# Kernel optimization log

Hardware: AMD Instinct MI355X
Metric: run time of the kernel (lower is better)

The kernel has to match this reference:

```python
import jax, jax.numpy as jnp
from jax import lax
import numpy as np

VOCAB, IN_DIM, MEM_DIM, SEQ = 100000, 256, 512, 2048
PAD = 0


def setup_inputs() -> dict:
    key = jax.random.key(0)
    k = jax.random.split(key, 7)
    emb = jax.random.normal(k[0], (VOCAB, IN_DIM), dtype=jnp.float32)
    emb = emb.at[PAD].set(0.0)  # padding_idx row is zero
    s_ih = 1.0 / np.sqrt(IN_DIM)
    s_hh = 1.0 / np.sqrt(MEM_DIM)
    return {
        "linputs": jax.random.randint(k[1], (SEQ,), 0, VOCAB, dtype=jnp.int64),
        "rinputs": jax.random.randint(k[2], (SEQ,), 0, VOCAB, dtype=jnp.int64),
        "emb": emb,
        "W_ih": jax.random.normal(k[3], (4 * MEM_DIM, IN_DIM), dtype=jnp.float32) * s_ih,
        "W_hh": jax.random.normal(k[4], (4 * MEM_DIM, MEM_DIM), dtype=jnp.float32) * s_hh,
        "b_ih": jax.random.normal(k[5], (4 * MEM_DIM,), dtype=jnp.float32) * s_hh,
        "b_hh": jax.random.normal(k[6], (4 * MEM_DIM,), dtype=jnp.float32) * s_hh,
    }


def _lstm_last_h(x_seq, W_ih, W_hh, b):
    # x_seq: [S, in_dim]. Returns h_T [mem_dim]. PyTorch gate order: i, f, g, o.
    H = W_hh.shape[1]
    # precompute input projections for all timesteps (one big GEMM)
    xp = x_seq @ W_ih.T + b  # [S, 4H]
    def step(carry, xg):
        h, c = carry
        gates = xg + h @ W_hh.T  # [4H]
        i = jax.nn.sigmoid(gates[:H])
        f = jax.nn.sigmoid(gates[H:2 * H])
        g = jnp.tanh(gates[2 * H:3 * H])
        o = jax.nn.sigmoid(gates[3 * H:])
        c = f * c + i * g
        h = o * jnp.tanh(c)
        return (h, c), None
    init = (jnp.zeros((H,), x_seq.dtype), jnp.zeros((H,), x_seq.dtype))
    (h, _), _ = lax.scan(step, init, xp)
    return h


def reference(linputs, rinputs, emb, W_ih, W_hh, b_ih, b_hh):
    b = b_ih + b_hh
    lx = emb[linputs]  # [S, in_dim]
    rx = emb[rinputs]
    lh = _lstm_last_h(lx, W_ih, W_hh, b)
    rh = _lstm_last_h(rx, W_ih, W_hh, b)
    return jnp.exp(-jnp.sum(jnp.abs(lh - rh)))
```

## Files before the change

kernel.cpp:

```cpp
#include <hip/hip_runtime.h>
#include <hip/hip_bf16.h>

#define SEQL  2048
#define IND   256
#define MEMD  512
#define G4    2048
#define NWG   16
#define VOCABN 100000

typedef __attribute__((ext_vector_type(4))) unsigned uintx4;

__device__ __forceinline__ unsigned short f2bf(float f) {
  unsigned u = __float_as_uint(f);
  u += 0x7fffu + ((u >> 16) & 1u);
  return (unsigned short)(u >> 16);
}
__device__ __forceinline__ float bf2f(unsigned b) {
  return __uint_as_float(b << 16);
}

template <int CTRL>
__device__ __forceinline__ float dpp_fold_add(float v) {
  int x = __builtin_amdgcn_update_dpp(0, __float_as_int(v), CTRL, 0xf, 0xf, true);
  return v + __int_as_float(x);
}

__global__ void init_k(unsigned* __restrict__ hbuf) {
  int i = blockIdx.x * blockDim.x + threadIdx.x;
  if (i < 2 * 2 * MEMD) hbuf[i] = 0u;
}

__global__ __launch_bounds__(256) void xp_gemm(
    const int* __restrict__ lin, const int* __restrict__ rin,
    const float* __restrict__ emb, const float* __restrict__ W_ih,
    const float* __restrict__ b_ih, const float* __restrict__ b_hh,
    unsigned short* __restrict__ xp) {
  __shared__ float As[64][68];
  __shared__ float Bs[64][68];
  const int s = blockIdx.z;
  const int* ids = (s == 0) ? lin : rin;
  const int t0 = blockIdx.x * 64;
  const int n0 = blockIdx.y * 64;
  const int tid = threadIdx.x;
  const int tx = tid & 15, ty = tid >> 4;

  float acc[4][4];
#pragma unroll
  for (int i = 0; i < 4; ++i)
#pragma unroll
    for (int j = 0; j < 4; ++j) acc[i][j] = 0.f;

  for (int kc = 0; kc < IND; kc += 64) {
#pragma unroll
    for (int j = 0; j < 4; ++j) {
      int fi  = tid + 256 * j;
      int row = fi >> 4;
      int c4  = fi & 15;
      int id  = ids[t0 + row];
      id = max(0, min(id, VOCABN - 1));
      const float4 va = *(const float4*)(emb + (size_t)id * IND + kc + c4 * 4);
      As[c4 * 4 + 0][row] = va.x; As[c4 * 4 + 1][row] = va.y;
      As[c4 * 4 + 2][row] = va.z; As[c4 * 4 + 3][row] = va.w;
      const float4 vb = *(const float4*)(W_ih + (size_t)(n0 + row) * IND + kc + c4 * 4);
      Bs[c4 * 4 + 0][row] = vb.x; Bs[c4 * 4 + 1][row] = vb.y;
      Bs[c4 * 4 + 2][row] = vb.z; Bs[c4 * 4 + 3][row] = vb.w;
    }
    __syncthreads();
#pragma unroll 8
    for (int k = 0; k < 64; ++k) {
      const float4 a = *(const float4*)&As[k][tx * 4];
      const float4 b = *(const float4*)&Bs[k][ty * 4];
      acc[0][0] = fmaf(a.x, b.x, acc[0][0]); acc[0][1] = fmaf(a.x, b.y, acc[0][1]);
      acc[0][2] = fmaf(a.x, b.z, acc[0][2]); acc[0][3] = fmaf(a.x, b.w, acc[0][3]);
      acc[1][0] = fmaf(a.y, b.x, acc[1][0]); acc[1][1] = fmaf(a.y, b.y, acc[1][1]);
      acc[1][2] = fmaf(a.y, b.z, acc[1][2]); acc[1][3] = fmaf(a.y, b.w, acc[1][3]);
      acc[2][0] = fmaf(a.z, b.x, acc[2][0]); acc[2][1] = fmaf(a.z, b.y, acc[2][1]);
      acc[2][2] = fmaf(a.z, b.z, acc[2][2]); acc[2][3] = fmaf(a.z, b.w, acc[2][3]);
      acc[3][0] = fmaf(a.w, b.x, acc[3][0]); acc[3][1] = fmaf(a.w, b.y, acc[3][1]);
      acc[3][2] = fmaf(a.w, b.z, acc[3][2]); acc[3][3] = fmaf(a.w, b.w, acc[3][3]);
    }
    __syncthreads();
  }
#pragma unroll
  for (int ri = 0; ri < 4; ++ri) {
#pragma unroll
    for (int bj = 0; bj < 4; ++bj) {
      int t = t0 + tx * 4 + ri;
      int n = n0 + ty * 4 + bj;
      float v = acc[ri][bj] + b_ih[n] + b_hh[n];
      int w = (n & 511) >> 5;
      int gate = n >> 9;
      int hd = n & 31;
      int pos = w * 128 + hd * 4 + gate;
      xp[((size_t)s * SEQL + t) * G4 + pos] = f2bf(v);
    }
  }
}

__global__ __launch_bounds__(512) void lstm_rec(
    const float* __restrict__ W_hh,
    const unsigned short* __restrict__ xp,
    unsigned* __restrict__ hbuf) {
  __shared__ float hlds[16 * 36];
  const int blk = blockIdx.x;
  const int s = blk & 1;
  const int w = blk >> 1;
  const int tid = threadIdx.x;
  const int lane = tid & 63;
  const int wv = tid >> 6;
  const int cg = tid & 15;
  const int rg = tid >> 4;

  float wreg[4][32];
#pragma unroll
  for (int g = 0; g < 4; ++g) {
    const float* src = W_hh + ((size_t)g * MEMD + w * 32 + rg) * MEMD + cg * 32;
#pragma unroll
    for (int q = 0; q < 8; ++q) {
      const float4 v = *(const float4*)(src + q * 4);
      wreg[g][q * 4 + 0] = v.x; wreg[g][q * 4 + 1] = v.y;
      wreg[g][q * 4 + 2] = v.z; wreg[g][q * 4 + 3] = v.w;
    }
  }

  unsigned* hbase = hbuf + s * (2 * MEMD);
  const unsigned short* xq0 = xp + (size_t)s * SEQL * G4 + w * 128 + rg * 4;
  float cst = 0.f;

  ushort4 xg_cur = *(const ushort4*)xq0;

  for (int t = 0; t < SEQL; ++t) {
    ushort4 xg_next;
    {
      int tn = (t + 1 < SEQL) ? t + 1 : t;
      xg_next = *(const ushort4*)(xq0 + (size_t)tn * G4);
    }

    if (wv == 0) {
      const unsigned* hr = hbase + (t & 1) * MEMD;
      unsigned v[8];
      const unsigned want = (unsigned)t;
      int guard = 0;
      for (;;) {
#pragma unroll
        for (int j = 0; j < 8; ++j)
          v[j] = __hip_atomic_load(hr + lane + 64 * j, __ATOMIC_RELAXED,
                                   __HIP_MEMORY_SCOPE_AGENT);
        bool good = true;
#pragma unroll
        for (int j = 0; j < 8; ++j) good &= ((v[j] >> 16) == want);
        if (__all(good)) break;
        if (++guard > (1 << 20)) break;
      }
#pragma unroll
      for (int j = 0; j < 8; ++j) {
        int wj = lane + 64 * j;
        hlds[(wj >> 5) * 36 + (wj & 31)] = bf2f(v[j] & 0xffffu);
      }
    }
    __syncthreads();

    float hreg[32];
#pragma unroll
    for (int q = 0; q < 8; ++q) {
      const float4 hv = *(const float4*)&hlds[cg * 36 + q * 4];
      hreg[q * 4 + 0] = hv.x; hreg[q * 4 + 1] = hv.y;
      hreg[q * 4 + 2] = hv.z; hreg[q * 4 + 3] = hv.w;
    }
    float part[4] = {0.f, 0.f, 0.f, 0.f};
#pragma unroll
    for (int kk = 0; kk < 32; ++kk) {
#pragma unroll
      for (int g = 0; g < 4; ++g)
        part[g] = fmaf(wreg[g][kk], hreg[kk], part[g]);
    }
#pragma unroll
    for (int g = 0; g < 4; ++g) {
      part[g] = dpp_fold_add<0xB1>(part[g]);
      part[g] = dpp_fold_add<0x4E>(part[g]);
      part[g] = dpp_fold_add<0x141>(part[g]);
      part[g] = dpp_fold_add<0x140>(part[g]);
    }

    float gi = part[0] + bf2f(xg_cur.x);
    float gf = part[1] + bf2f(xg_cur.y);
    float gg = part[2] + bf2f(xg_cur.z);
    float go = part[3] + bf2f(xg_cur.w);
    float i_ = 1.f / (1.f + __expf(-gi));
    float f_ = 1.f / (1.f + __expf(-gf));
    float ggc = fminf(fmaxf(gg, -15.f), 15.f);
    float e2 = __expf(-2.f * ggc);
    float g_ = (1.f - e2) / (1.f + e2);
    float o_ = 1.f / (1.f + __expf(-go));
    cst = f_ * cst + i_ * g_;
    float cc = fminf(fmaxf(cst, -15.f), 15.f);
    float e2c = __expf(-2.f * cc);
    float th = (1.f - e2c) / (1.f + e2c);
    float h_ = o_ * th;

    unsigned pw = (((unsigned)(t + 1)) << 16) | (unsigned)f2bf(h_);
    unsigned q1 = __shfl(pw, 16, 64);
    unsigned q2 = __shfl(pw, 32, 64);
    unsigned q3 = __shfl(pw, 48, 64);
    if (lane == 0) {
      uintx4 val;
      val.x = pw; val.y = q1; val.z = q2; val.w = q3;
      unsigned long long addr =
          (unsigned long long)(hbase + ((t + 1) & 1) * MEMD + w * 32 + wv * 4);
      asm volatile("global_store_dwordx4 %0, %1, off sc0 sc1"
                   :: "v"(addr), "v"(val) : "memory");
    }
    xg_cur = xg_next;
  }
}

__global__ __launch_bounds__(512) void finish_k(const unsigned* __restrict__ hbuf,
                                                float* __restrict__ out) {
  const int tid = threadIdx.x;
  float l = bf2f(hbuf[tid] & 0xffffu);
  float r = bf2f(hbuf[2 * MEMD + tid] & 0xffffu);
  float d = fabsf(l - r);
#pragma unroll
  for (int m = 32; m >= 1; m >>= 1) d += __shfl_xor(d, m, 64);
  __shared__ float wsum[8];
  if ((tid & 63) == 0) wsum[tid >> 6] = d;
  __syncthreads();
  if (tid == 0) {
    float sum = 0.f;
#pragma unroll
    for (int i = 0; i < 8; ++i) sum += wsum[i];
    out[0] = expf(-sum);
  }
}

extern "C" void kernel_launch(void* const* d_in, const int* in_sizes, int n_in,
                              void* d_out, int out_size, void* d_ws, size_t ws_size,
                              hipStream_t stream) {
  const int*   lin  = (const int*)d_in[0];
  const int*   rin  = (const int*)d_in[1];
  const float* emb  = (const float*)d_in[2];
  const float* W_ih = (const float*)d_in[3];
  const float* W_hh = (const float*)d_in[4];
  const float* b_ih = (const float*)d_in[5];
  const float* b_hh = (const float*)d_in[6];
  float* out = (float*)d_out;

  unsigned char* ws = (unsigned char*)d_ws;
  unsigned short* xp = (unsigned short*)ws;
  unsigned* hbuf = (unsigned*)(ws + (size_t)2 * SEQL * G4 * sizeof(unsigned short));

  hipLaunchKernelGGL(init_k, dim3(2), dim3(1024), 0, stream, hbuf);
  hipLaunchKernelGGL(xp_gemm, dim3(SEQL / 64, G4 / 64, 2), dim3(256), 0, stream,
                     lin, rin, emb, W_ih, b_ih, b_hh, xp);
  hipLaunchKernelGGL(lstm_rec, dim3(2 * NWG), dim3(512), 0, stream, W_hh, xp, hbuf);
  hipLaunchKernelGGL(finish_k, dim3(1), dim3(512), 0, stream, hbuf, out);
}
```

Baseline: 3.786 ms.

## Switch recurrent state and weights to fp16 with packed fdot2 matvec

Stores the input projections and the exchanged hidden state as fp16 instead of bf16, and packs the W_hh register slice into half2 pairs so the recurrent matvec uses v_dot2 (fdot2) with fp32 accumulation. The hidden-state poll now uses two dwordx4 loads per lane instead of eight scalar atomics. The LDS staging buffer holds packed half pairs, and launch bounds request two blocks per SM. The intent is fewer instructions and fewer registers on the serial per-step critical path, at the cost of fp16 range and precision for the weights and gate inputs.

```diff
diff --git a/kernel.cpp b/kernel.cpp
--- a/kernel.cpp
+++ b/kernel.cpp
@@ -9,14 +9,14 @@
 #define VOCABN 100000
 
 typedef __attribute__((ext_vector_type(4))) unsigned uintx4;
-
-__device__ __forceinline__ unsigned short f2bf(float f) {
-  unsigned u = __float_as_uint(f);
-  u += 0x7fffu + ((u >> 16) & 1u);
-  return (unsigned short)(u >> 16);
-}
-__device__ __forceinline__ float bf2f(unsigned b) {
-  return __uint_as_float(b << 16);
+typedef __attribute__((ext_vector_type(2))) _Float16 half2v;
+
+__device__ __forceinline__ unsigned short f2h_bits(float f) {
+  _Float16 h = (_Float16)f;
+  return __builtin_bit_cast(unsigned short, h);
+}
+__device__ __forceinline__ float h2f(unsigned bits) {
+  return (float)__builtin_bit_cast(_Float16, (unsigned short)(bits & 0xffffu));
 }
 
 template <int CTRL>
@@ -92,16 +92,16 @@
       int gate = n >> 9;
       int hd = n & 31;
       int pos = w * 128 + hd * 4 + gate;
-      xp[((size_t)s * SEQL + t) * G4 + pos] = f2bf(v);
-    }
-  }
-}
-
-__global__ __launch_bounds__(512) void lstm_rec(
+      xp[((size_t)s * SEQL + t) * G4 + pos] = f2h_bits(v);
+    }
+  }
+}
+
+__global__ __launch_bounds__(512, 2) void lstm_rec(
     const float* __restrict__ W_hh,
     const unsigned short* __restrict__ xp,
     unsigned* __restrict__ hbuf) {
-  __shared__ float hlds[16 * 36];
+  __shared__ unsigned hlds[16 * 20];
   const int blk = blockIdx.x;
   const int s = blk & 1;
   const int w = blk >> 1;
@@ -111,15 +111,17 @@
   const int cg = tid & 15;
   const int rg = tid >> 4;
 
-  float wreg[4][32];
+  half2v wreg[4][16];
 #pragma unroll
   for (int g = 0; g < 4; ++g) {
     const float* src = W_hh + ((size_t)g * MEMD + w * 32 + rg) * MEMD + cg * 32;
 #pragma unroll
     for (int q = 0; q < 8; ++q) {
       const float4 v = *(const float4*)(src + q * 4);
-      wreg[g][q * 4 + 0] = v.x; wreg[g][q * 4 + 1] = v.y;
-      wreg[g][q * 4 + 2] = v.z; wreg[g][q * 4 + 3] = v.w;
+      half2v p0; p0.x = (_Float16)v.x; p0.y = (_Float16)v.y;
+      half2v p1; p1.x = (_Float16)v.z; p1.y = (_Float16)v.w;
+      wreg[g][q * 2 + 0] = p0;
+      wreg[g][q * 2 + 1] = p1;
     }
   }
 
@@ -137,42 +139,54 @@
     }
 
     if (wv == 0) {
-      const unsigned* hr = hbase + (t & 1) * MEMD;
-      unsigned v[8];
+      const unsigned* hr = hbase + (t & 1) * MEMD + 8 * lane;
+      unsigned long long a0 = (unsigned long long)hr;
+      unsigned long long a1 = (unsigned long long)(hr + 4);
+      uintx4 va, vb;
       const unsigned want = (unsigned)t;
       int guard = 0;
       for (;;) {
-#pragma unroll
-        for (int j = 0; j < 8; ++j)
-          v[j] = __hip_atomic_load(hr + lane + 64 * j, __ATOMIC_RELAXED,
-                                   __HIP_MEMORY_SCOPE_AGENT);
-        bool good = true;
-#pragma unroll
-        for (int j = 0; j < 8; ++j) good &= ((v[j] >> 16) == want);
+        asm volatile(
+            "global_load_dwordx4 %0, %2, off sc0 sc1\n\t"
+            "global_load_dwordx4 %1, %3, off sc0 sc1\n\t"
+            "s_waitcnt vmcnt(0)"
+            : "=&v"(va), "=&v"(vb)
+            : "v"(a0), "v"(a1)
+            : "memory");
+        bool good = (va.x >> 16) == want && (va.y >> 16) == want &&
+                    (va.z >> 16) == want && (va.w >> 16) == want &&
+                    (vb.x >> 16) == want && (vb.y >> 16) == want &&
+                    (vb.z >> 16) == want && (vb.w >> 16) == want;
         if (__all(good)) break;
-        if (++guard > (1 << 20)) break;
+        if (++guard > (1 << 16)) break;
       }
-#pragma unroll
-      for (int j = 0; j < 8; ++j) {
-        int wj = lane + 64 * j;
-        hlds[(wj >> 5) * 36 + (wj & 31)] = bf2f(v[j] & 0xffffu);
+      uintx4 pk;
+      pk.x = (va.x & 0xffffu) | (va.y << 16);
+      pk.y = (va.z & 0xffffu) | (va.w << 16);
+      pk.z = (vb.x & 0xffffu) | (vb.y << 16);
+      pk.w = (vb.z & 0xffffu) | (vb.w << 16);
+      *(uintx4*)&hlds[(lane >> 2) * 20 + (lane & 3) * 4] = pk;
+    }
+    __syncthreads();
+
+    half2v hp[16];
+    {
+      const uintx4* hq = (const uintx4*)&hlds[cg * 20];
+#pragma unroll
+      for (int q = 0; q < 4; ++q) {
+        uintx4 u = hq[q];
+        hp[q * 4 + 0] = __builtin_bit_cast(half2v, u.x);
+        hp[q * 4 + 1] = __builtin_bit_cast(half2v, u.y);
+        hp[q * 4 + 2] = __builtin_bit_cast(half2v, u.z);
+        hp[q * 4 + 3] = __builtin_bit_cast(half2v, u.w);
       }
     }
-    __syncthreads();
-
-    float hreg[32];
-#pragma unroll
-    for (int q = 0; q < 8; ++q) {
-      const float4 hv = *(const float4*)&hlds[cg * 36 + q * 4];
-      hreg[q * 4 + 0] = hv.x; hreg[q * 4 + 1] = hv.y;
-      hreg[q * 4 + 2] = hv.z; hreg[q * 4 + 3] = hv.w;
-    }
     float part[4] = {0.f, 0.f, 0.f, 0.f};
 #pragma unroll
-    for (int kk = 0; kk < 32; ++kk) {
+    for (int p = 0; p < 16; ++p) {
 #pragma unroll
       for (int g = 0; g < 4; ++g)
-        part[g] = fmaf(wreg[g][kk], hreg[kk], part[g]);
+        part[g] = __builtin_amdgcn_fdot2(wreg[g][p], hp[p], part[g], false);
     }
 #pragma unroll
     for (int g = 0; g < 4; ++g) {
@@ -182,10 +196,10 @@
       part[g] = dpp_fold_add<0x140>(part[g]);
     }
 
-    float gi = part[0] + bf2f(xg_cur.x);
-    float gf = part[1] + bf2f(xg_cur.y);
-    float gg = part[2] + bf2f(xg_cur.z);
-    float go = part[3] + bf2f(xg_cur.w);
+    float gi = part[0] + h2f(xg_cur.x);
+    float gf = part[1] + h2f(xg_cur.y);
+    float gg = part[2] + h2f(xg_cur.z);
+    float go = part[3] + h2f(xg_cur.w);
     float i_ = 1.f / (1.f + __expf(-gi));
     float f_ = 1.f / (1.f + __expf(-gf));
     float ggc = fminf(fmaxf(gg, -15.f), 15.f);
@@ -198,7 +212,7 @@
     float th = (1.f - e2c) / (1.f + e2c);
     float h_ = o_ * th;
 
-    unsigned pw = (((unsigned)(t + 1)) << 16) | (unsigned)f2bf(h_);
+    unsigned pw = (((unsigned)(t + 1)) << 16) | (unsigned)f2h_bits(h_);
     unsigned q1 = __shfl(pw, 16, 64);
     unsigned q2 = __shfl(pw, 32, 64);
     unsigned q3 = __shfl(pw, 48, 64);
@@ -217,8 +231,8 @@
 __global__ __launch_bounds__(512) void finish_k(const unsigned* __restrict__ hbuf,
                                                 float* __restrict__ out) {
   const int tid = threadIdx.x;
-  float l = bf2f(hbuf[tid] & 0xffffu);
-  float r = bf2f(hbuf[2 * MEMD + tid] & 0xffffu);
+  float l = h2f(hbuf[tid]);
+  float r = h2f(hbuf[2 * MEMD + tid]);
   float d = fabsf(l - r);
 #pragma unroll
   for (int m = 32; m >= 1; m >>= 1) d += __shfl_xor(d, m, 64);
```

Result: faster. 3.661 ms (-3.3%).
